# Kernel tuning notes

Measured on AMD Instinct MI355X. Metric: run time of the kernel, lower is better.

Reference implementation:

```python
import jax, jax.numpy as jnp
import numpy as np

B, S, D, H = 4, 2048, 1024, 16
HD = D // H


def setup_inputs() -> dict:
    key = jax.random.key(0)
    ks = jax.random.split(key, 10)
    x = jax.random.normal(ks[0], (B, S, D), dtype=jnp.float32)
    mask = jnp.zeros((B, 1, 1, S), dtype=jnp.float32)  # 1 = masked, 0 = keep
    sc = 1.0 / np.sqrt(D)
    wq = jax.random.normal(ks[1], (D, D), dtype=jnp.float32) * sc
    wk = jax.random.normal(ks[2], (D, D), dtype=jnp.float32) * sc
    wv = jax.random.normal(ks[3], (D, D), dtype=jnp.float32) * sc
    wo = jax.random.normal(ks[4], (D, D), dtype=jnp.float32) * sc
    bq = jnp.zeros((D,), jnp.float32)
    bk = jnp.zeros((D,), jnp.float32)
    bv = jnp.zeros((D,), jnp.float32)
    bo = jnp.zeros((D,), jnp.float32)
    return {"x": x, "mask": mask, "wq": wq, "bq": bq, "wk": wk, "bk": bk,
            "wv": wv, "bv": bv, "wo": wo, "bo": bo}


def _split_heads(t):
    # (B, S, D) -> (B, H, S, HD)
    return t.reshape(B, -1, H, HD).transpose(0, 2, 1, 3)


def reference(x, mask, wq, bq, wk, bk, wv, bv, wo, bo):
    q = _split_heads(x @ wq + bq)
    k = _split_heads(x @ wk + bk)
    v = _split_heads(x @ wv + bv)
    # scaled dot-product attention (TF tutorial convention: mask*-1e9 added)
    scores = jnp.einsum("bhqd,bhkd->bhqk", q, k) / jnp.sqrt(jnp.float32(HD))
    scores = scores + mask * -1e9
    attn_weights = jax.nn.softmax(scores, axis=-1)  # (B, H, Sq, Sk)
    attn = jnp.einsum("bhqk,bhkd->bhqd", attn_weights, v)
    attn = attn.transpose(0, 2, 1, 3).reshape(B, -1, D)
    out = attn @ wo + bo
    return out, attn_weights
```

## Files before the change

kernel.cpp:

```cpp
#include <hip/hip_runtime.h>
#include <hip/hip_bf16.h>

#define S_LEN  2048
#define DMODEL 1024
#define NHEAD  16
#define HDIM   64
#define BSZ    4

#define C_SCORE  0.18033688f
#define C_MASK  -1.4426950e9f

typedef __bf16 bf16_t;
typedef __bf16 bf16x8 __attribute__((ext_vector_type(8)));
typedef __bf16 bf16x4 __attribute__((ext_vector_type(4)));
typedef float  f32x4  __attribute__((ext_vector_type(4)));

typedef __attribute__((address_space(1))) void as1_void;
typedef __attribute__((address_space(3))) void as3_void;

__device__ __forceinline__ f32x4 mfma16(bf16x8 a, bf16x8 b, f32x4 c) {
    return __builtin_amdgcn_mfma_f32_16x16x32_bf16(a, b, c, 0, 0, 0);
}

__global__ __launch_bounds__(256) void cvt_all(const float* __restrict__ x,
                                               bf16_t* __restrict__ xb,
                                               const float* __restrict__ w0,
                                               const float* __restrict__ w1,
                                               const float* __restrict__ w2,
                                               const float* __restrict__ w3,
                                               bf16_t* __restrict__ wT) {
    __shared__ bf16_t t[64][65];
    const int bid = blockIdx.x;
    if (bid < 4096) {
        const int i0 = bid * 256 + threadIdx.x;
        #pragma unroll
        for (int rep = 0; rep < 2; ++rep) {
            const int i = i0 + rep * 1048576;
            float4 v = ((const float4*)x)[i];
            bf16x4 tv = { (bf16_t)v.x, (bf16_t)v.y, (bf16_t)v.z, (bf16_t)v.w };
            ((bf16x4*)xb)[i] = tv;
        }
        return;
    }
    const int wb = bid - 4096;
    const int wsel = wb >> 8;
    const float* w = wsel == 0 ? w0 : (wsel == 1 ? w1 : (wsel == 2 ? w2 : w3));
    bf16_t* wTo = wT + (size_t)wsel * DMODEL * DMODEL;
    const int rb = wb & 255;
    const int bx = (rb & 15) * 64, by = (rb >> 4) * 64;
    const int tx = threadIdx.x & 63, ty = threadIdx.x >> 6;
    #pragma unroll
    for (int rr = 0; rr < 64; rr += 4)
        t[tx][rr + ty] = (bf16_t)w[(size_t)(bx + rr + ty) * DMODEL + by + tx];
    __syncthreads();
    #pragma unroll
    for (int rr = 0; rr < 64; rr += 4)
        wTo[(size_t)(by + rr + ty) * DMODEL + bx + tx] = t[rr + ty][tx];
}

template <int MODE>
__global__ __launch_bounds__(256) void gemm_bt(const bf16_t* __restrict__ A,
                                               const bf16_t* __restrict__ Bt,
                                               const float* __restrict__ b0,
                                               const float* __restrict__ b1,
                                               const float* __restrict__ b2,
                                               bf16_t* __restrict__ o0,
                                               bf16_t* __restrict__ o1,
                                               bf16_t* __restrict__ o2,
                                               float* __restrict__ of) {
    constexpr int GK = 1024;
    __shared__ __attribute__((aligned(16))) bf16_t smem_ab[8704];
    bf16_t* As = smem_ab;
    bf16_t* Bs = smem_ab + 4096;

    const int tid  = threadIdx.x;
    const int wave = tid >> 6, lane = tid & 63;
    const int col16 = lane & 15, g = lane >> 4;
    const int wr = wave >> 1, wc = wave & 1;
    const int bn0 = blockIdx.x * 128, bm0 = blockIdx.y * 128;

    const int r4 = tid >> 2;
    const int c8 = (tid & 3) * 8;

    f32x4 acc[4][4] = {};

    for (int k0 = 0; k0 < GK; k0 += 32) {
        __syncthreads();
        #pragma unroll
        for (int i = 0; i < 2; ++i) {
            __builtin_amdgcn_global_load_lds(
                (const as1_void*)(A + (size_t)(bm0 + i * 64 + r4) * GK + k0 + c8),
                (as3_void*)(As + (i * 64 + wave * 16) * 32), 16, 0, 0);
            __builtin_amdgcn_global_load_lds(
                (const as1_void*)(Bt + (size_t)(bn0 + i * 64 + r4) * GK + k0 + c8),
                (as3_void*)(Bs + (i * 64 + wave * 16) * 32), 16, 0, 0);
        }
        __syncthreads();

        bf16x8 af[4], bfr[4];
        #pragma unroll
        for (int i = 0; i < 4; ++i) {
            af[i]  = *(const bf16x8*)(As + (wr * 64 + i * 16 + col16) * 32 + g * 8);
            bfr[i] = *(const bf16x8*)(Bs + (wc * 64 + i * 16 + col16) * 32 + g * 8);
        }
        #pragma unroll
        for (int mi = 0; mi < 4; ++mi)
            #pragma unroll
            for (int ni = 0; ni < 4; ++ni)
                acc[mi][ni] = mfma16(af[mi], bfr[ni], acc[mi][ni]);
    }

    if (MODE == 0) {
        const int proj = bn0 >> 10;
        const int brow = bm0 >> 11;
        const int s0 = bm0 & 2047;
        const int n1b = bn0 & 1023;

        if (proj == 2) {
            __syncthreads();
            #pragma unroll
            for (int p = 0; p < 2; ++p) {
                if (p) __syncthreads();
                if (wc == p) {
                    #pragma unroll
                    for (int ni = 0; ni < 4; ++ni) {
                        const float bv = b2[n1b + p * 64 + ni * 16 + col16];
                        #pragma unroll
                        for (int mi = 0; mi < 4; ++mi) {
                            bf16x4 pv;
                            #pragma unroll
                            for (int r = 0; r < 4; ++r) pv[r] = (bf16_t)(acc[mi][ni][r] + bv);
                            *(bf16x4*)&smem_ab[(ni * 16 + col16) * 136 + wr * 64 + mi * 16 + g * 4] = pv;
                        }
                    }
                }
                __syncthreads();
                const int h2 = (n1b + p * 64) >> 6;
                bf16_t* vout = o2 + (((size_t)brow * NHEAD + h2) * HDIM) * S_LEN + s0;
                #pragma unroll
                for (int j = 0; j < 4; ++j) {
                    const int unit = j * 256 + tid;
                    const int row = unit >> 4;
                    const int cu = (unit & 15) * 8;
                    bf16x8 v = *(const bf16x8*)&smem_ab[row * 136 + cu];
                    *(bf16x8*)(vout + (size_t)row * S_LEN + cu) = v;
                }
            }
            return;
        }

        const float* bias = proj == 0 ? b0 : b1;
        bf16_t* outp      = proj == 0 ? o0 : o1;
        __syncthreads();
        #pragma unroll
        for (int p = 0; p < 2; ++p) {
            if (p) __syncthreads();
            if (wc == p) {
                #pragma unroll
                for (int ni = 0; ni < 4; ++ni) {
                    const float bv = bias[n1b + p * 64 + ni * 16 + col16];
                    #pragma unroll
                    for (int mi = 0; mi < 4; ++mi)
                        #pragma unroll
                        for (int r = 0; r < 4; ++r)
                            smem_ab[(wr * 64 + mi * 16 + g * 4 + r) * 64 + ni * 16 + col16] =
                                (bf16_t)(acc[mi][ni][r] + bv);
                }
            }
            __syncthreads();
            const int h2 = (n1b + p * 64) >> 6;
            bf16_t* qout = outp + (((size_t)brow * NHEAD + h2) * S_LEN + s0) * HDIM;
            #pragma unroll
            for (int pass = 0; pass < 4; ++pass) {
                const int idx = pass * 256 + tid;
                bf16x8 v = *(const bf16x8*)&smem_ab[idx * 8];
                *(bf16x8*)(qout + (size_t)idx * 8) = v;
            }
        }
        return;
    }

    {
        float* smem_f = (float*)smem_ab;
        float bvr[4];
        #pragma unroll
        for (int ni = 0; ni < 4; ++ni)
            bvr[ni] = b0[bn0 + wc * 64 + ni * 16 + col16];
        __syncthreads();
        #pragma unroll
        for (int c = 0; c < 8; ++c) {
            if (c) __syncthreads();
            if (wr == (c >> 2)) {
                const int mi = c & 3;
                #pragma unroll
                for (int ni = 0; ni < 4; ++ni)
                    #pragma unroll
                    for (int r = 0; r < 4; ++r)
                        smem_f[(g * 4 + r) * 132 + wc * 64 + ni * 16 + col16] =
                            acc[mi][ni][r] + bvr[ni];
            }
            __syncthreads();
            #pragma unroll
            for (int k2 = 0; k2 < 2; ++k2) {
                const int idx = k2 * 256 + tid;
                const int row = idx >> 5, u = idx & 31;
                f32x4 v = *(const f32x4*)&smem_f[row * 132 + u * 4];
                *(f32x4*)(of + (size_t)(bm0 + c * 16 + row) * DMODEL + bn0 + u * 4) = v;
            }
        }
    }
}

__global__ __launch_bounds__(512, 4) void attn_fused(const bf16_t* __restrict__ Q,
                                                     const bf16_t* __restrict__ K,
                                                     const bf16_t* __restrict__ Vt,
                                                     const float* __restrict__ mask,
                                                     float* __restrict__ attnW,
                                                     bf16_t* __restrict__ ctx) {
    __shared__ __attribute__((aligned(16))) char smem[73728];
    bf16_t (*KsA)[128][64] = (bf16_t(*)[128][64])smem;
    bf16_t (*Ks)[64][64]   = (bf16_t(*)[64][64])smem;
    bf16_t (*Vs)[64][64]   = (bf16_t(*)[64][64])(smem + 16384);
    float  (*Pl)[16][64]   = (float(*)[16][64])(smem + 32768);
    float*  Ml             = (float*)(smem + 65536);

    const int tid = threadIdx.x, wave = tid >> 6, lane = tid & 63;
    const int col16 = lane & 15, g = lane >> 4;
    const int r7 = col16 & 7;

    const int lin = blockIdx.x;
    const int logical = (lin & 7) * 64 + (lin >> 3);
    const int bh = logical >> 3, pp = logical & 7;
    const int b = bh >> 4, h = bh & 15;
    const int qA = pp * 256 + wave * 16;
    const int qB = pp * 256 + 128 + wave * 16;

    const bf16_t* Qb = Q + (size_t)bh * S_LEN * HDIM;
    const bf16_t* Kb = K + (size_t)bh * S_LEN * HDIM;
    const bf16_t* Vb = Vt + (size_t)bh * HDIM * S_LEN;
    const float* mp = mask + (size_t)b * S_LEN;

    {
        f32x4 v = ((const f32x4*)mp)[tid];
        #pragma unroll
        for (int r = 0; r < 4; ++r) v[r] *= C_MASK;
        *(f32x4*)(&Ml[tid * 4]) = v;
    }

    const int srow  = lane >> 3;
    const int sunit = (lane & 7) ^ srow;

    auto stageA = [&](int buf, int it) {
        const int kk0 = it << 7;
        #pragma unroll
        for (int i2 = 0; i2 < 2; ++i2) {
            const int i = wave * 2 + i2;
            __builtin_amdgcn_global_load_lds(
                (const as1_void*)(Kb + (size_t)(kk0 + i * 8 + srow) * HDIM + sunit * 8),
                (as3_void*)(&KsA[buf][i * 8][0]), 16, 0, 0);
        }
    };
    auto stageK = [&](int buf, int it) {
        const int kk0 = it << 6;
        __builtin_amdgcn_global_load_lds(
            (const as1_void*)(Kb + (size_t)(kk0 + wave * 8 + srow) * HDIM + sunit * 8),
            (as3_void*)(&Ks[buf][wave * 8][0]), 16, 0, 0);
    };
    auto stageV = [&](int buf, int it) {
        const int kk0 = it << 6;
        __builtin_amdgcn_global_load_lds(
            (const as1_void*)(Vb + (size_t)(wave * 8 + srow) * S_LEN + kk0 + sunit * 8),
            (as3_void*)(&Vs[buf][wave * 8][0]), 16, 0, 0);
    };
    auto kfrag = [&](int buf, int nj, int kh) {
        return *(const bf16x8*)(&Ks[buf][nj * 16 + col16][(((kh * 4 + g) ^ r7) * 8)]);
    };
    auto vfrag = [&](int buf, int nd, int kh) {
        return *(const bf16x8*)(&Vs[buf][nd * 16 + col16][(((kh * 4 + g) ^ r7) * 8)]);
    };

    bf16x8 qa0[2], qa1[2];
    #pragma unroll
    for (int kh = 0; kh < 2; ++kh) {
        qa0[kh] = *(const bf16x8*)(Qb + (size_t)(qA + col16) * HDIM + kh * 32 + g * 8);
        qa1[kh] = *(const bf16x8*)(Qb + (size_t)(qB + col16) * HDIM + kh * 32 + g * 8);
    }

    f32x4 lacc0 = {}, lacc1 = {};
    stageA(0, 0);
    __syncthreads();

    for (int it = 0; it < 16; ++it) {
        const int kk0 = it << 7, cur = it & 1;
        if (it < 15) stageA(cur ^ 1, it + 1);
        #pragma unroll
        for (int nj = 0; nj < 8; ++nj) {
            const f32x4 mvr = *(const f32x4*)(&Ml[kk0 + nj * 16 + g * 4]);
            const bf16x8 kf0 = *(const bf16x8*)(&KsA[cur][nj * 16 + col16][((g ^ r7) * 8)]);
            const bf16x8 kf1 = *(const bf16x8*)(&KsA[cur][nj * 16 + col16][(((4 + g) ^ r7) * 8)]);
            f32x4 t0 = {0.f, 0.f, 0.f, 0.f}, u0 = {0.f, 0.f, 0.f, 0.f};
            t0 = mfma16(kf0, qa0[0], t0);
            t0 = mfma16(kf1, qa0[1], t0);
            u0 = mfma16(kf0, qa1[0], u0);
            u0 = mfma16(kf1, qa1[1], u0);
            #pragma unroll
            for (int r = 0; r < 4; ++r) {
                lacc0[r] += exp2f(fmaf(t0[r], C_SCORE, mvr[r]));
                lacc1[r] += exp2f(fmaf(u0[r], C_SCORE, mvr[r]));
            }
        }
        asm volatile("s_waitcnt vmcnt(0)" ::: "memory");
        __builtin_amdgcn_sched_barrier(0);
        __builtin_amdgcn_s_barrier();
    }

    float crow0, crow1;
    {
        float lr0 = (lacc0[0] + lacc0[1]) + (lacc0[2] + lacc0[3]);
        lr0 += __shfl_xor(lr0, 16);
        lr0 += __shfl_xor(lr0, 32);
        crow0 = -__log2f(lr0);
        float lr1 = (lacc1[0] + lacc1[1]) + (lacc1[2] + lacc1[3]);
        lr1 += __shfl_xor(lr1, 16);
        lr1 += __shfl_xor(lr1, 32);
        crow1 = -__log2f(lr1);
    }

    f32x4 o0[4] = {}, o1[4] = {};
    float* awA = attnW + ((size_t)bh * S_LEN + qA) * S_LEN;
    float* awB = attnW + ((size_t)bh * S_LEN + qB) * S_LEN;

    stageK(0, 0);
    stageV(0, 0);
    asm volatile("s_waitcnt vmcnt(0)" ::: "memory");
    __builtin_amdgcn_sched_barrier(0);
    __builtin_amdgcn_s_barrier();

    for (int it = 0; it < 32; ++it) {
        const int kk0 = it << 6, cur = it & 1;
        if (it < 31) { stageK(cur ^ 1, it + 1); stageV(cur ^ 1, it + 1); }
        __builtin_amdgcn_sched_barrier(0);
        f32x4 mvr[4];
        #pragma unroll
        for (int nj = 0; nj < 4; ++nj)
            mvr[nj] = *(const f32x4*)(&Ml[kk0 + nj * 16 + g * 4]);

        #pragma unroll
        for (int nj = 0; nj < 4; ++nj) {
            const bf16x8 kf0 = kfrag(cur, nj, 0);
            const bf16x8 kf1 = kfrag(cur, nj, 1);
            f32x4 s0 = {0.f, 0.f, 0.f, 0.f};
            s0 = mfma16(kf0, qa0[0], s0);
            s0 = mfma16(kf1, qa0[1], s0);
            f32x4 pn0;
            #pragma unroll
            for (int r = 0; r < 4; ++r)
                pn0[r] = exp2f(fmaf(s0[r], C_SCORE, mvr[nj][r] + crow0));
            *(f32x4*)(&Pl[wave][col16][(((nj * 4 + g) ^ r7) * 4)]) = pn0;
        }
        #pragma unroll
        for (int j = 0; j < 4; ++j) {
            const int row = j * 4 + (lane >> 4);
            const int u = lane & 15;
            const f32x4 v = *(const f32x4*)(&Pl[wave][row][((u ^ (row & 7)) * 4)]);
            __builtin_nontemporal_store(v, (f32x4*)(awA + (size_t)row * S_LEN + kk0 + u * 4));
        }
        #pragma unroll
        for (int kh = 0; kh < 2; ++kh) {
            const int u0i = kh * 8 + g * 2;
            const f32x4 a0 = *(const f32x4*)(&Pl[wave][col16][((u0i ^ r7) * 4)]);
            const f32x4 a1 = *(const f32x4*)(&Pl[wave][col16][(((u0i + 1) ^ r7) * 4)]);
            bf16x8 pa;
            #pragma unroll
            for (int j = 0; j < 4; ++j) {
                pa[j]     = (bf16_t)a0[j];
                pa[4 + j] = (bf16_t)a1[j];
            }
            #pragma unroll
            for (int nd = 0; nd < 4; ++nd)
                o0[nd] = mfma16(vfrag(cur, nd, kh), pa, o0[nd]);
        }

        #pragma unroll
        for (int nj = 0; nj < 4; ++nj) {
            const bf16x8 kf0 = kfrag(cur, nj, 0);
            const bf16x8 kf1 = kfrag(cur, nj, 1);
            f32x4 s0 = {0.f, 0.f, 0.f, 0.f};
            s0 = mfma16(kf0, qa1[0], s0);
            s0 = mfma16(kf1, qa1[1], s0);
            f32x4 pn0;
            #pragma unroll
            for (int r = 0; r < 4; ++r)
                pn0[r] = exp2f(fmaf(s0[r], C_SCORE, mvr[nj][r] + crow1));
            *(f32x4*)(&Pl[wave][col16][(((nj * 4 + g) ^ r7) * 4)]) = pn0;
        }
        #pragma unroll
        for (int j = 0; j < 4; ++j) {
            const int row = j * 4 + (lane >> 4);
            const int u = lane & 15;
            const f32x4 v = *(const f32x4*)(&Pl[wave][row][((u ^ (row & 7)) * 4)]);
            __builtin_nontemporal_store(v, (f32x4*)(awB + (size_t)row * S_LEN + kk0 + u * 4));
        }
        #pragma unroll
        for (int kh = 0; kh < 2; ++kh) {
            const int u0i = kh * 8 + g * 2;
            const f32x4 a0 = *(const f32x4*)(&Pl[wave][col16][((u0i ^ r7) * 4)]);
            const f32x4 a1 = *(const f32x4*)(&Pl[wave][col16][(((u0i + 1) ^ r7) * 4)]);
            bf16x8 pa;
            #pragma unroll
            for (int j = 0; j < 4; ++j) {
                pa[j]     = (bf16_t)a0[j];
                pa[4 + j] = (bf16_t)a1[j];
            }
            #pragma unroll
            for (int nd = 0; nd < 4; ++nd)
                o1[nd] = mfma16(vfrag(cur, nd, kh), pa, o1[nd]);
        }

        asm volatile("s_waitcnt vmcnt(8)" ::: "memory");
        __builtin_amdgcn_sched_barrier(0);
        __builtin_amdgcn_s_barrier();
    }

    {
        bf16_t* cpA = ctx + ((size_t)b * S_LEN + qA + col16) * DMODEL + h * HDIM;
        bf16_t* cpB = ctx + ((size_t)b * S_LEN + qB + col16) * DMODEL + h * HDIM;
        #pragma unroll
        for (int nd = 0; nd < 4; ++nd) {
            bf16x4 cv0, cv1;
            #pragma unroll
            for (int r = 0; r < 4; ++r) {
                cv0[r] = (bf16_t)o0[nd][r];
                cv1[r] = (bf16_t)o1[nd][r];
            }
            *(bf16x4*)(cpA + nd * 16 + g * 4) = cv0;
            *(bf16x4*)(cpB + nd * 16 + g * 4) = cv1;
        }
    }
}

extern "C" void kernel_launch(void* const* d_in, const int* in_sizes, int n_in,
                              void* d_out, int out_size, void* d_ws, size_t ws_size,
                              hipStream_t stream) {
    const float* x    = (const float*)d_in[0];
    const float* mask = (const float*)d_in[1];
    const float* wq   = (const float*)d_in[2];
    const float* bq   = (const float*)d_in[3];
    const float* wk   = (const float*)d_in[4];
    const float* bk   = (const float*)d_in[5];
    const float* wv   = (const float*)d_in[6];
    const float* bv   = (const float*)d_in[7];
    const float* wo   = (const float*)d_in[8];
    const float* bo   = (const float*)d_in[9];

    const size_t nX = (size_t)BSZ * S_LEN * DMODEL;
    const size_t nW = (size_t)DMODEL * DMODEL;

    char* ws = (char*)d_ws;
    size_t off = 0;
    bf16_t* xb     = (bf16_t*)(ws + off); off += nX * 2;
    bf16_t* wqkvT  = (bf16_t*)(ws + off); off += 3 * nW * 2;
    bf16_t* woT    = (bf16_t*)(ws + off); off += nW * 2;
    bf16_t* qbh    = (bf16_t*)(ws + off); off += nX * 2;
    bf16_t* kbh    = (bf16_t*)(ws + off); off += nX * 2;
    bf16_t* vtb    = (bf16_t*)(ws + off); off += nX * 2;
    bf16_t* ctx    = (bf16_t*)(ws + off); off += nX * 2;
    if (ws_size < off) return;

    float* outp  = (float*)d_out;
    float* attnW = outp + nX;

    cvt_all<<<5120, 256, 0, stream>>>(x, xb, wq, wk, wv, wo, wqkvT);

    gemm_bt<0><<<dim3(24, 64), 256, 0, stream>>>(xb, wqkvT, bq, bk, bv,
                                                 qbh, kbh, vtb, nullptr);

    attn_fused<<<512, 512, 0, stream>>>(qbh, kbh, vtb, mask, attnW, ctx);

    gemm_bt<2><<<dim3(8, 64), 256, 0, stream>>>(ctx, woT, bo, nullptr, nullptr,
                                                nullptr, nullptr, nullptr, outp);
}
```

Measured before the change: 369.0 us.

## Double-buffer GEMM LDS loads and remap workgroups across XCDs

The projection GEMMs now double-buffer their A/B tiles in shared memory, so the global-to-LDS load for the next K step is issued before the MFMAs on the current one, with one barrier per iteration instead of two. The grid is flattened to 1D and block indices are remapped so consecutive logical tiles land on the same XCD, which is meant to improve L2 reuse. Shared memory per block roughly doubles, which may lower occupancy. The GEMMs are only part of a runtime dominated by attention and the attention-weights write.

```diff
diff --git a/kernel.cpp b/kernel.cpp
--- a/kernel.cpp
+++ b/kernel.cpp
@@ -69,23 +69,26 @@
                                                bf16_t* __restrict__ o2,
                                                float* __restrict__ of) {
     constexpr int GK = 1024;
-    __shared__ __attribute__((aligned(16))) bf16_t smem_ab[8704];
-    bf16_t* As = smem_ab;
-    bf16_t* Bs = smem_ab + 4096;
+    constexpr int NBX = (MODE == 0) ? 24 : 8;
+    constexpr int NWG = (MODE == 0) ? 1536 : 512;
+    __shared__ __attribute__((aligned(16))) bf16_t smem_ab[16384];
 
     const int tid  = threadIdx.x;
     const int wave = tid >> 6, lane = tid & 63;
     const int col16 = lane & 15, g = lane >> 4;
     const int wr = wave >> 1, wc = wave & 1;
-    const int bn0 = blockIdx.x * 128, bm0 = blockIdx.y * 128;
+
+    const int lin = blockIdx.x;
+    const int logical = (lin & 7) * (NWG / 8) + (lin >> 3);
+    const int bn0 = (logical % NBX) * 128;
+    const int bm0 = (logical / NBX) * 128;
 
     const int r4 = tid >> 2;
     const int c8 = (tid & 3) * 8;
 
-    f32x4 acc[4][4] = {};
-
-    for (int k0 = 0; k0 < GK; k0 += 32) {
-        __syncthreads();
+    auto stage = [&](int buf, int k0) {
+        bf16_t* As = smem_ab + buf * 8192;
+        bf16_t* Bs = As + 4096;
         #pragma unroll
         for (int i = 0; i < 2; ++i) {
             __builtin_amdgcn_global_load_lds(
@@ -95,19 +98,31 @@
                 (const as1_void*)(Bt + (size_t)(bn0 + i * 64 + r4) * GK + k0 + c8),
                 (as3_void*)(Bs + (i * 64 + wave * 16) * 32), 16, 0, 0);
         }
-        __syncthreads();
+    };
+
+    f32x4 acc[4][4] = {};
+
+    stage(0, 0);
+    __syncthreads();
+
+    for (int t = 0; t < 32; ++t) {
+        if (t < 31) stage((t + 1) & 1, (t + 1) * 32);
+        __builtin_amdgcn_sched_barrier(0);
+        bf16_t* Ac = smem_ab + (t & 1) * 8192;
+        bf16_t* Bc = Ac + 4096;
 
         bf16x8 af[4], bfr[4];
         #pragma unroll
         for (int i = 0; i < 4; ++i) {
-            af[i]  = *(const bf16x8*)(As + (wr * 64 + i * 16 + col16) * 32 + g * 8);
-            bfr[i] = *(const bf16x8*)(Bs + (wc * 64 + i * 16 + col16) * 32 + g * 8);
+            af[i]  = *(const bf16x8*)(Ac + (wr * 64 + i * 16 + col16) * 32 + g * 8);
+            bfr[i] = *(const bf16x8*)(Bc + (wc * 64 + i * 16 + col16) * 32 + g * 8);
         }
         #pragma unroll
         for (int mi = 0; mi < 4; ++mi)
             #pragma unroll
             for (int ni = 0; ni < 4; ++ni)
                 acc[mi][ni] = mfma16(af[mi], bfr[ni], acc[mi][ni]);
+        __syncthreads();
     }
 
     if (MODE == 0) {
@@ -117,7 +132,6 @@
         const int n1b = bn0 & 1023;
 
         if (proj == 2) {
-            __syncthreads();
             #pragma unroll
             for (int p = 0; p < 2; ++p) {
                 if (p) __syncthreads();
@@ -151,7 +165,6 @@
 
         const float* bias = proj == 0 ? b0 : b1;
         bf16_t* outp      = proj == 0 ? o0 : o1;
-        __syncthreads();
         #pragma unroll
         for (int p = 0; p < 2; ++p) {
             if (p) __syncthreads();
@@ -186,7 +199,6 @@
         #pragma unroll
         for (int ni = 0; ni < 4; ++ni)
             bvr[ni] = b0[bn0 + wc * 64 + ni * 16 + col16];
-        __syncthreads();
         #pragma unroll
         for (int c = 0; c < 8; ++c) {
             if (c) __syncthreads();
@@ -472,11 +484,11 @@
 
     cvt_all<<<5120, 256, 0, stream>>>(x, xb, wq, wk, wv, wo, wqkvT);
 
-    gemm_bt<0><<<dim3(24, 64), 256, 0, stream>>>(xb, wqkvT, bq, bk, bv,
-                                                 qbh, kbh, vtb, nullptr);
+    gemm_bt<0><<<1536, 256, 0, stream>>>(xb, wqkvT, bq, bk, bv,
+                                         qbh, kbh, vtb, nullptr);
 
     attn_fused<<<512, 512, 0, stream>>>(qbh, kbh, vtb, mask, attnW, ctx);
 
-    gemm_bt<2><<<dim3(8, 64), 256, 0, stream>>>(ctx, woT, bo, nullptr, nullptr,
-                                                nullptr, nullptr, nullptr, outp);
+    gemm_bt<2><<<512, 256, 0, stream>>>(ctx, woT, bo, nullptr, nullptr,
+                                        nullptr, nullptr, nullptr, outp);
 }
```

Result: no change. 374.9 us (+1.6%).
